# Performance work log

Measured on AMD Instinct MI355X. Metric: run time of the kernel, lower is better.

## Reference

```python
import jax, jax.numpy as jnp
import numpy as np

ALPHA = 0.2  # LeakyReLU negative slope
NEG_PAD = jnp.float32(-2**31)
N, IN_F, OUT_F = 8192, 512, 64


def setup_inputs() -> dict:
    key = jax.random.key(0)
    k1, k2, k3, k4 = jax.random.split(key, 4)
    h = jax.random.normal(k1, (N, IN_F), dtype=jnp.float32)
    adj = jax.random.randint(k2, (N, N), 0, 2, dtype=jnp.int32)
    # xavier_uniform with gain=1.414
    gain = 1.414
    limW = gain * np.sqrt(6.0 / (IN_F + OUT_F))
    W = jax.random.uniform(k3, (IN_F, OUT_F), dtype=jnp.float32, minval=-limW, maxval=limW)
    lima = gain * np.sqrt(6.0 / (2 * OUT_F + 1))
    a = jax.random.uniform(k4, (2 * OUT_F, 1), dtype=jnp.float32, minval=-lima, maxval=lima)
    return {"h": h, "adj": adj, "W": W, "a": a}


def reference(h, adj, W, a):
    Wh = h @ W                                   # [N, F']
    Wh1 = Wh @ a[:OUT_F, :]                      # [N, 1]
    Wh2 = Wh @ a[OUT_F:, :]                      # [N, 1]
    e = jax.nn.leaky_relu(Wh1 + Wh2.T, negative_slope=ALPHA)  # [N, N]
    attention = jnp.where(adj > 0, e, NEG_PAD)
    attention = jax.nn.softmax(attention, axis=1)
    # dropout in eval mode -> identity
    h_prime = attention @ Wh                     # [N, F']
    return jax.nn.elu(h_prime)                   # concat=True branch
```

## Files before the change

### kernel.cpp

```cpp
#include <hip/hip_runtime.h>
#include <cstdint>
#include <cstddef>

#define LRALPHA 0.2f

typedef _Float16 half8 __attribute__((ext_vector_type(8)));
typedef float f32x4 __attribute__((ext_vector_type(4)));

__global__ __launch_bounds__(256) void k1_wh(
    const float* __restrict__ h, const float* __restrict__ W, const float* __restrict__ a,
    _Float16* __restrict__ whT, float* __restrict__ wh1, float* __restrict__ wh2)
{
  __shared__ __align__(16) float h_lds[32][34];
  __shared__ __align__(16) float w_lds[32][64];
  __shared__ __align__(16) _Float16 whT_l[64][32];

  const int t = threadIdx.x;
  const int tx = t & 15, ty = t >> 4;
  const int i0 = blockIdx.x * 32;

  const int hrow = t >> 3, hk4 = (t & 7) * 4;
  const int wk = t >> 3, wc = (t & 7) * 8;

  float acc00 = 0, acc01 = 0, acc02 = 0, acc03 = 0;
  float acc10 = 0, acc11 = 0, acc12 = 0, acc13 = 0;

  float4 hv  = *reinterpret_cast<const float4*>(&h[(size_t)(i0 + hrow) * 512 + hk4]);
  float4 wv0 = *reinterpret_cast<const float4*>(&W[(size_t)wk * 64 + wc]);
  float4 wv1 = *reinterpret_cast<const float4*>(&W[(size_t)wk * 64 + wc + 4]);

  for (int k0 = 0; k0 < 512; k0 += 32) {
    h_lds[hk4 + 0][hrow] = hv.x;
    h_lds[hk4 + 1][hrow] = hv.y;
    h_lds[hk4 + 2][hrow] = hv.z;
    h_lds[hk4 + 3][hrow] = hv.w;
    *reinterpret_cast<float4*>(&w_lds[wk][wc])     = wv0;
    *reinterpret_cast<float4*>(&w_lds[wk][wc + 4]) = wv1;
    __syncthreads();
    if (k0 + 32 < 512) {
      hv  = *reinterpret_cast<const float4*>(&h[(size_t)(i0 + hrow) * 512 + k0 + 32 + hk4]);
      wv0 = *reinterpret_cast<const float4*>(&W[(size_t)(k0 + 32 + wk) * 64 + wc]);
      wv1 = *reinterpret_cast<const float4*>(&W[(size_t)(k0 + 32 + wk) * 64 + wc + 4]);
    }
#pragma unroll
    for (int kk = 0; kk < 32; ++kk) {
      float2 av = *reinterpret_cast<const float2*>(&h_lds[kk][ty * 2]);
      float4 bv = *reinterpret_cast<const float4*>(&w_lds[kk][tx * 4]);
      acc00 += av.x * bv.x; acc01 += av.x * bv.y; acc02 += av.x * bv.z; acc03 += av.x * bv.w;
      acc10 += av.y * bv.x; acc11 += av.y * bv.y; acc12 += av.y * bv.z; acc13 += av.y * bv.w;
    }
    __syncthreads();
  }

  const float a10 = a[tx * 4 + 0], a11 = a[tx * 4 + 1], a12 = a[tx * 4 + 2], a13 = a[tx * 4 + 3];
  const float a20 = a[64 + tx * 4 + 0], a21 = a[64 + tx * 4 + 1], a22 = a[64 + tx * 4 + 2], a23 = a[64 + tx * 4 + 3];
  float s1_0 = acc00 * a10 + acc01 * a11 + acc02 * a12 + acc03 * a13;
  float s1_1 = acc10 * a10 + acc11 * a11 + acc12 * a12 + acc13 * a13;
  float s2_0 = acc00 * a20 + acc01 * a21 + acc02 * a22 + acc03 * a23;
  float s2_1 = acc10 * a20 + acc11 * a21 + acc12 * a22 + acc13 * a23;
#pragma unroll
  for (int m = 1; m < 16; m <<= 1) {
    s1_0 += __shfl_xor(s1_0, m); s1_1 += __shfl_xor(s1_1, m);
    s2_0 += __shfl_xor(s2_0, m); s2_1 += __shfl_xor(s2_1, m);
  }
  if (tx == 0) {
    wh1[i0 + ty * 2 + 0] = s1_0; wh1[i0 + ty * 2 + 1] = s1_1;
    wh2[i0 + ty * 2 + 0] = s2_0; wh2[i0 + ty * 2 + 1] = s2_1;
  }

  whT_l[tx * 4 + 0][ty * 2 + 0] = (_Float16)acc00;
  whT_l[tx * 4 + 1][ty * 2 + 0] = (_Float16)acc01;
  whT_l[tx * 4 + 2][ty * 2 + 0] = (_Float16)acc02;
  whT_l[tx * 4 + 3][ty * 2 + 0] = (_Float16)acc03;
  whT_l[tx * 4 + 0][ty * 2 + 1] = (_Float16)acc10;
  whT_l[tx * 4 + 1][ty * 2 + 1] = (_Float16)acc11;
  whT_l[tx * 4 + 2][ty * 2 + 1] = (_Float16)acc12;
  whT_l[tx * 4 + 3][ty * 2 + 1] = (_Float16)acc13;
  __syncthreads();
  {
    const int c = t >> 2, r8 = (t & 3) * 8;
    half8 v = *reinterpret_cast<const half8*>(&whT_l[c][r8]);
    *reinterpret_cast<half8*>(&whT[(size_t)c * 8192 + i0 + r8]) = v;
  }
}

__global__ __launch_bounds__(256) void k1b_max(const float* __restrict__ wh2,
                                               float* __restrict__ G)
{
  const int t = threadIdx.x;
  float m = -1e30f;
  for (int i = t; i < 8192; i += 256) m = fmaxf(m, wh2[i]);
#pragma unroll
  for (int mask = 32; mask >= 1; mask >>= 1) m = fmaxf(m, __shfl_xor(m, mask));
  __shared__ float wm[4];
  if ((t & 63) == 0) wm[t >> 6] = m;
  __syncthreads();
  if (t == 0) G[0] = fmaxf(fmaxf(wm[0], wm[1]), fmaxf(wm[2], wm[3]));
}

__global__ __launch_bounds__(512) void k2_attn(
    const int* __restrict__ adj, const _Float16* __restrict__ whT,
    const float* __restrict__ wh1, const float* __restrict__ wh2,
    const float* __restrict__ Gp, float* __restrict__ out)
{
  __shared__ __align__(16) unsigned char smraw[16384];
  __shared__ float denom_s[64];
  _Float16* P = reinterpret_cast<_Float16*>(smraw);
  float* O = reinterpret_cast<float*>(smraw);

  const int t = threadIdx.x;
  const int g = t >> 8;
  const int tg = t & 255;
  const int lane = t & 63;
  const int wg = (t >> 6) & 3;
  const int i0 = blockIdx.x * 32;

  if (t < 64) denom_s[t] = 0.f;

  const float Gv = Gp[0];
  const int prow = tg >> 3;
  const int pc8 = tg & 7;
  const float w1r = wh1[i0 + prow];
  const float mx = w1r + Gv;
  const float mh = fmaxf(mx, LRALPHA * mx);
  const int* adj_row = adj + (size_t)(i0 + prow) * 8192 + pc8 * 8;
  const float* wh2o = wh2 + pc8 * 8;

  const int rt = wg >> 1, cp = wg & 1;
  const int arow = rt * 16 + (lane & 15);
  const int kgrp = lane >> 4;
  const _Float16* bbase = whT + (size_t)(cp * 32 + (lane & 15)) * 8192 + kgrp * 8;

  f32x4 acc0 = {0.f, 0.f, 0.f, 0.f}, acc1 = {0.f, 0.f, 0.f, 0.f};

  int4 na0, na1; float4 nw0, nw1;
  {
    const int j0 = g * 64;
    na0 = *reinterpret_cast<const int4*>(adj_row + j0);
    na1 = *reinterpret_cast<const int4*>(adj_row + j0 + 4);
    nw0 = *reinterpret_cast<const float4*>(wh2o + j0);
    nw1 = *reinterpret_cast<const float4*>(wh2o + j0 + 4);
  }
  __syncthreads();

  for (int ci = 0; ci < 64; ++ci) {
    const int j0 = (2 * ci + g) * 64;
    const int buf = ci & 1;
    const int4 a0 = na0, a1 = na1;
    const float4 w0 = nw0, w1v = nw1;

    const _Float16* bp = bbase + j0;
    half8 bf00 = *reinterpret_cast<const half8*>(bp);
    half8 bf01 = *reinterpret_cast<const half8*>(bp + (size_t)16 * 8192);
    half8 bf10 = *reinterpret_cast<const half8*>(bp + 32);
    half8 bf11 = *reinterpret_cast<const half8*>(bp + (size_t)16 * 8192 + 32);

    if (ci < 63) {
      const int jn = (2 * ci + 2 + g) * 64;
      na0 = *reinterpret_cast<const int4*>(adj_row + jn);
      na1 = *reinterpret_cast<const int4*>(adj_row + jn + 4);
      nw0 = *reinterpret_cast<const float4*>(wh2o + jn);
      nw1 = *reinterpret_cast<const float4*>(wh2o + jn + 4);
    }

    half8 pv;
    float ps = 0.f;
#define DO_E(e, AV, WV) { float s_ = w1r + (WV); s_ = fmaxf(s_, LRALPHA * s_); \
    float p_ = ((AV) > 0) ? __expf(s_ - mh) : 0.f; ps += p_; pv[e] = (_Float16)p_; }
    DO_E(0, a0.x, w0.x)  DO_E(1, a0.y, w0.y)  DO_E(2, a0.z, w0.z)  DO_E(3, a0.w, w0.w)
    DO_E(4, a1.x, w1v.x) DO_E(5, a1.y, w1v.y) DO_E(6, a1.z, w1v.z) DO_E(7, a1.w, w1v.w)
#undef DO_E

    float r = ps;
    r += __shfl_xor(r, 1); r += __shfl_xor(r, 2); r += __shfl_xor(r, 4);
    if (pc8 == 0) denom_s[g * 32 + prow] += r;

    {
      const int chunk = pc8 ^ (prow & 7);
      *reinterpret_cast<half8*>(&P[(((g << 1) | buf) << 11) + (prow << 6) + (chunk << 3)]) = pv;
    }
    __syncthreads();

    const int base = (((g << 1) | buf) << 11) + (arow << 6);
    const int cA0 = (kgrp ^ (arow & 7)) << 3;
    const int cA1 = ((4 + kgrp) ^ (arow & 7)) << 3;
    half8 af0 = *reinterpret_cast<const half8*>(&P[base + cA0]);
    half8 af1 = *reinterpret_cast<const half8*>(&P[base + cA1]);
    acc0 = __builtin_amdgcn_mfma_f32_16x16x32_f16(af0, bf00, acc0, 0, 0, 0);
    acc1 = __builtin_amdgcn_mfma_f32_16x16x32_f16(af0, bf01, acc1, 0, 0, 0);
    acc0 = __builtin_amdgcn_mfma_f32_16x16x32_f16(af1, bf10, acc0, 0, 0, 0);
    acc1 = __builtin_amdgcn_mfma_f32_16x16x32_f16(af1, bf11, acc1, 0, 0, 0);
  }

  __syncthreads();
  const int orow = rt * 16 + kgrp * 4;
  const int ocol = cp * 32 + (lane & 15);
  if (g == 0) {
#pragma unroll
    for (int q = 0; q < 4; ++q) {
      O[(orow + q) * 64 + ocol]      = acc0[q];
      O[(orow + q) * 64 + ocol + 16] = acc1[q];
    }
  }
  __syncthreads();
  if (g == 1) {
#pragma unroll
    for (int q = 0; q < 4; ++q) {
      O[(orow + q) * 64 + ocol]      += acc0[q];
      O[(orow + q) * 64 + ocol + 16] += acc1[q];
    }
  }
  __syncthreads();
  {
    const int row = t >> 4, c4 = (t & 15) * 4;
    const float d = denom_s[row] + denom_s[32 + row];
    const float inv = 1.0f / d;
    float4 v = *reinterpret_cast<const float4*>(&O[row * 64 + c4]);
    float4 o;
    o.x = v.x * inv; o.y = v.y * inv; o.z = v.z * inv; o.w = v.w * inv;
    o.x = o.x > 0.f ? o.x : __expf(o.x) - 1.f;
    o.y = o.y > 0.f ? o.y : __expf(o.y) - 1.f;
    o.z = o.z > 0.f ? o.z : __expf(o.z) - 1.f;
    o.w = o.w > 0.f ? o.w : __expf(o.w) - 1.f;
    *reinterpret_cast<float4*>(&out[(size_t)(i0 + row) * 64 + c4]) = o;
  }
}

extern "C" void kernel_launch(void* const* d_in, const int* in_sizes, int n_in,
                              void* d_out, int out_size, void* d_ws, size_t ws_size,
                              hipStream_t stream) {
  const float* h   = (const float*)d_in[0];
  const int*   adj = (const int*)d_in[1];
  const float* W   = (const float*)d_in[2];
  const float* a   = (const float*)d_in[3];
  float* out = (float*)d_out;

  char* ws = (char*)d_ws;
  _Float16* whT = (_Float16*)ws;
  float* wh1 = (float*)(ws + (1 << 20));
  float* wh2 = (float*)(ws + (1 << 20) + 32768);
  float* G   = (float*)(ws + (1 << 20) + 65536);

  k1_wh<<<dim3(256), dim3(256), 0, stream>>>(h, W, a, whT, wh1, wh2);
  k1b_max<<<dim3(1), dim3(256), 0, stream>>>(wh2, G);
  k2_attn<<<dim3(256), dim3(512), 0, stream>>>(adj, whT, wh1, wh2, G, out);
}
```

Baseline: 106.8 us.

## Compute attention probabilities directly in MFMA operand layout, split K across waves

```diff
diff --git a/kernel.cpp b/kernel.cpp
--- a/kernel.cpp
+++ b/kernel.cpp
@@ -98,126 +98,116 @@
   if (t == 0) G[0] = fmaxf(fmaxf(wm[0], wm[1]), fmaxf(wm[2], wm[3]));
 }
 
-__global__ __launch_bounds__(512) void k2_attn(
+__global__ __launch_bounds__(256) void k2_attn(
     const int* __restrict__ adj, const _Float16* __restrict__ whT,
     const float* __restrict__ wh1, const float* __restrict__ wh2,
     const float* __restrict__ Gp, float* __restrict__ out)
 {
-  __shared__ __align__(16) unsigned char smraw[16384];
-  __shared__ float denom_s[64];
-  _Float16* P = reinterpret_cast<_Float16*>(smraw);
-  float* O = reinterpret_cast<float*>(smraw);
+  __shared__ __align__(16) float Osm[4][16][64];
+  __shared__ float Dsm[4][16];
 
   const int t = threadIdx.x;
-  const int g = t >> 8;
-  const int tg = t & 255;
   const int lane = t & 63;
-  const int wg = (t >> 6) & 3;
-  const int i0 = blockIdx.x * 32;
-
-  if (t < 64) denom_s[t] = 0.f;
+  const int w = t >> 6;
+  const int c = lane & 15;
+  const int ks = lane >> 4;
+  const int i0 = blockIdx.x * 16;
 
   const float Gv = Gp[0];
-  const int prow = tg >> 3;
-  const int pc8 = tg & 7;
-  const float w1r = wh1[i0 + prow];
+  const float w1r = wh1[i0 + c];
   const float mx = w1r + Gv;
   const float mh = fmaxf(mx, LRALPHA * mx);
-  const int* adj_row = adj + (size_t)(i0 + prow) * 8192 + pc8 * 8;
-  const float* wh2o = wh2 + pc8 * 8;
-
-  const int rt = wg >> 1, cp = wg & 1;
-  const int arow = rt * 16 + (lane & 15);
-  const int kgrp = lane >> 4;
-  const _Float16* bbase = whT + (size_t)(cp * 32 + (lane & 15)) * 8192 + kgrp * 8;
-
-  f32x4 acc0 = {0.f, 0.f, 0.f, 0.f}, acc1 = {0.f, 0.f, 0.f, 0.f};
-
-  int4 na0, na1; float4 nw0, nw1;
-  {
-    const int j0 = g * 64;
-    na0 = *reinterpret_cast<const int4*>(adj_row + j0);
-    na1 = *reinterpret_cast<const int4*>(adj_row + j0 + 4);
-    nw0 = *reinterpret_cast<const float4*>(wh2o + j0);
-    nw1 = *reinterpret_cast<const float4*>(wh2o + j0 + 4);
+
+  const int*      adjp = adj + (size_t)(i0 + c) * 8192 + w * 2048 + ks * 8;
+  const float*    wh2p = wh2 + w * 2048 + ks * 8;
+  const _Float16* bp0  = whT + (size_t)c * 8192 + w * 2048 + ks * 8;
+  const _Float16* bp1  = bp0 + (size_t)16 * 8192;
+  const _Float16* bp2  = bp0 + (size_t)32 * 8192;
+  const _Float16* bp3  = bp0 + (size_t)48 * 8192;
+
+  f32x4 acc0 = {0.f,0.f,0.f,0.f}, acc1 = {0.f,0.f,0.f,0.f};
+  f32x4 acc2 = {0.f,0.f,0.f,0.f}, acc3 = {0.f,0.f,0.f,0.f};
+  float ps = 0.f;
+
+  int4 Aa0, Aa1, Ba0, Ba1;
+  float4 Aw0, Aw1, Bw0, Bw1;
+  half8 Ab0, Ab1, Ab2, Ab3, Bb0, Bb1, Bb2, Bb3;
+
+#define LOADSET(P, CI) do { const int jj_ = (CI) * 32;                          \
+    P##a0 = *reinterpret_cast<const int4*>(adjp + jj_);                         \
+    P##a1 = *reinterpret_cast<const int4*>(adjp + jj_ + 4);                     \
+    P##w0 = *reinterpret_cast<const float4*>(wh2p + jj_);                       \
+    P##w1 = *reinterpret_cast<const float4*>(wh2p + jj_ + 4);                   \
+    P##b0 = *reinterpret_cast<const half8*>(bp0 + jj_);                         \
+    P##b1 = *reinterpret_cast<const half8*>(bp1 + jj_);                         \
+    P##b2 = *reinterpret_cast<const half8*>(bp2 + jj_);                         \
+    P##b3 = *reinterpret_cast<const half8*>(bp3 + jj_); } while (0)
+
+#define BODY(P, NEXTCI) do {                                                    \
+    const int4 ca0 = P##a0, ca1 = P##a1;                                        \
+    const float4 cw0 = P##w0, cw1 = P##w1;                                      \
+    const half8 cb0 = P##b0, cb1 = P##b1, cb2 = P##b2, cb3 = P##b3;             \
+    if ((NEXTCI) < 64) LOADSET(P, NEXTCI);                                      \
+    half8 af;                                                                   \
+    { float s_ = w1r + cw0.x; s_ = fmaxf(s_, LRALPHA*s_);                       \
+      float p_ = (ca0.x > 0) ? __expf(s_ - mh) : 0.f; ps += p_; af[0] = (_Float16)p_; } \
+    { float s_ = w1r + cw0.y; s_ = fmaxf(s_, LRALPHA*s_);                       \
+      float p_ = (ca0.y > 0) ? __expf(s_ - mh) : 0.f; ps += p_; af[1] = (_Float16)p_; } \
+    { float s_ = w1r + cw0.z; s_ = fmaxf(s_, LRALPHA*s_);                       \
+      float p_ = (ca0.z > 0) ? __expf(s_ - mh) : 0.f; ps += p_; af[2] = (_Float16)p_; } \
+    { float s_ = w1r + cw0.w; s_ = fmaxf(s_, LRALPHA*s_);                       \
+      float p_ = (ca0.w > 0) ? __expf(s_ - mh) : 0.f; ps += p_; af[3] = (_Float16)p_; } \
+    { float s_ = w1r + cw1.x; s_ = fmaxf(s_, LRALPHA*s_);                       \
+      float p_ = (ca1.x > 0) ? __expf(s_ - mh) : 0.f; ps += p_; af[4] = (_Float16)p_; } \
+    { float s_ = w1r + cw1.y; s_ = fmaxf(s_, LRALPHA*s_);                       \
+      float p_ = (ca1.y > 0) ? __expf(s_ - mh) : 0.f; ps += p_; af[5] = (_Float16)p_; } \
+    { float s_ = w1r + cw1.z; s_ = fmaxf(s_, LRALPHA*s_);                       \
+      float p_ = (ca1.z > 0) ? __expf(s_ - mh) : 0.f; ps += p_; af[6] = (_Float16)p_; } \
+    { float s_ = w1r + cw1.w; s_ = fmaxf(s_, LRALPHA*s_);                       \
+      float p_ = (ca1.w > 0) ? __expf(s_ - mh) : 0.f; ps += p_; af[7] = (_Float16)p_; } \
+    acc0 = __builtin_amdgcn_mfma_f32_16x16x32_f16(af, cb0, acc0, 0, 0, 0);      \
+    acc1 = __builtin_amdgcn_mfma_f32_16x16x32_f16(af, cb1, acc1, 0, 0, 0);      \
+    acc2 = __builtin_amdgcn_mfma_f32_16x16x32_f16(af, cb2, acc2, 0, 0, 0);      \
+    acc3 = __builtin_amdgcn_mfma_f32_16x16x32_f16(af, cb3, acc3, 0, 0, 0);      \
+  } while (0)
+
+  LOADSET(A, 0);
+  LOADSET(B, 1);
+
+  for (int ci = 0; ci < 64; ci += 2) {
+    BODY(A, ci + 2);
+    BODY(B, ci + 3);
+  }
+#undef BODY
+#undef LOADSET
+
+  float r = ps;
+  r += __shfl_xor(r, 16);
+  r += __shfl_xor(r, 32);
+  if (ks == 0) Dsm[w][c] = r;
+
+#pragma unroll
+  for (int q = 0; q < 4; ++q) {
+    Osm[w][ks * 4 + q][ 0 + c] = acc0[q];
+    Osm[w][ks * 4 + q][16 + c] = acc1[q];
+    Osm[w][ks * 4 + q][32 + c] = acc2[q];
+    Osm[w][ks * 4 + q][48 + c] = acc3[q];
   }
   __syncthreads();
 
-  for (int ci = 0; ci < 64; ++ci) {
-    const int j0 = (2 * ci + g) * 64;
-    const int buf = ci & 1;
-    const int4 a0 = na0, a1 = na1;
-    const float4 w0 = nw0, w1v = nw1;
-
-    const _Float16* bp = bbase + j0;
-    half8 bf00 = *reinterpret_cast<const half8*>(bp);
-    half8 bf01 = *reinterpret_cast<const half8*>(bp + (size_t)16 * 8192);
-    half8 bf10 = *reinterpret_cast<const half8*>(bp + 32);
-    half8 bf11 = *reinterpret_cast<const half8*>(bp + (size_t)16 * 8192 + 32);
-
-    if (ci < 63) {
-      const int jn = (2 * ci + 2 + g) * 64;
-      na0 = *reinterpret_cast<const int4*>(adj_row + jn);
-      na1 = *reinterpret_cast<const int4*>(adj_row + jn + 4);
-      nw0 = *reinterpret_cast<const float4*>(wh2o + jn);
-      nw1 = *reinterpret_cast<const float4*>(wh2o + jn + 4);
-    }
-
-    half8 pv;
-    float ps = 0.f;
-#define DO_E(e, AV, WV) { float s_ = w1r + (WV); s_ = fmaxf(s_, LRALPHA * s_); \
-    float p_ = ((AV) > 0) ? __expf(s_ - mh) : 0.f; ps += p_; pv[e] = (_Float16)p_; }
-    DO_E(0, a0.x, w0.x)  DO_E(1, a0.y, w0.y)  DO_E(2, a0.z, w0.z)  DO_E(3, a0.w, w0.w)
-    DO_E(4, a1.x, w1v.x) DO_E(5, a1.y, w1v.y) DO_E(6, a1.z, w1v.z) DO_E(7, a1.w, w1v.w)
-#undef DO_E
-
-    float r = ps;
-    r += __shfl_xor(r, 1); r += __shfl_xor(r, 2); r += __shfl_xor(r, 4);
-    if (pc8 == 0) denom_s[g * 32 + prow] += r;
-
-    {
-      const int chunk = pc8 ^ (prow & 7);
-      *reinterpret_cast<half8*>(&P[(((g << 1) | buf) << 11) + (prow << 6) + (chunk << 3)]) = pv;
-    }
-    __syncthreads();
-
-    const int base = (((g << 1) | buf) << 11) + (arow << 6);
-    const int cA0 = (kgrp ^ (arow & 7)) << 3;
-    const int cA1 = ((4 + kgrp) ^ (arow & 7)) << 3;
-    half8 af0 = *reinterpret_cast<const half8*>(&P[base + cA0]);
-    half8 af1 = *reinterpret_cast<const half8*>(&P[base + cA1]);
-    acc0 = __builtin_amdgcn_mfma_f32_16x16x32_f16(af0, bf00, acc0, 0, 0, 0);
-    acc1 = __builtin_amdgcn_mfma_f32_16x16x32_f16(af0, bf01, acc1, 0, 0, 0);
-    acc0 = __builtin_amdgcn_mfma_f32_16x16x32_f16(af1, bf10, acc0, 0, 0, 0);
-    acc1 = __builtin_amdgcn_mfma_f32_16x16x32_f16(af1, bf11, acc1, 0, 0, 0);
-  }
-
-  __syncthreads();
-  const int orow = rt * 16 + kgrp * 4;
-  const int ocol = cp * 32 + (lane & 15);
-  if (g == 0) {
-#pragma unroll
-    for (int q = 0; q < 4; ++q) {
-      O[(orow + q) * 64 + ocol]      = acc0[q];
-      O[(orow + q) * 64 + ocol + 16] = acc1[q];
-    }
-  }
-  __syncthreads();
-  if (g == 1) {
-#pragma unroll
-    for (int q = 0; q < 4; ++q) {
-      O[(orow + q) * 64 + ocol]      += acc0[q];
-      O[(orow + q) * 64 + ocol + 16] += acc1[q];
-    }
-  }
-  __syncthreads();
   {
     const int row = t >> 4, c4 = (t & 15) * 4;
-    const float d = denom_s[row] + denom_s[32 + row];
+    float4 v0 = *reinterpret_cast<const float4*>(&Osm[0][row][c4]);
+    float4 v1 = *reinterpret_cast<const float4*>(&Osm[1][row][c4]);
+    float4 v2 = *reinterpret_cast<const float4*>(&Osm[2][row][c4]);
+    float4 v3 = *reinterpret_cast<const float4*>(&Osm[3][row][c4]);
+    const float d = Dsm[0][row] + Dsm[1][row] + Dsm[2][row] + Dsm[3][row];
     const float inv = 1.0f / d;
-    float4 v = *reinterpret_cast<const float4*>(&O[row * 64 + c4]);
     float4 o;
-    o.x = v.x * inv; o.y = v.y * inv; o.z = v.z * inv; o.w = v.w * inv;
+    o.x = (v0.x + v1.x + v2.x + v3.x) * inv;
+    o.y = (v0.y + v1.y + v2.y + v3.y) * inv;
+    o.z = (v0.z + v1.z + v2.z + v3.z) * inv;
+    o.w = (v0.w + v1.w + v2.w + v3.w) * inv;
     o.x = o.x > 0.f ? o.x : __expf(o.x) - 1.f;
     o.y = o.y > 0.f ? o.y : __expf(o.y) - 1.f;
     o.z = o.z > 0.f ? o.z : __expf(o.z) - 1.f;
@@ -243,5 +233,5 @@
 
   k1_wh<<<dim3(256), dim3(256), 0, stream>>>(h, W, a, whT, wh1, wh2);
   k1b_max<<<dim3(1), dim3(256), 0, stream>>>(wh2, G);
-  k2_attn<<<dim3(256), dim3(512), 0, stream>>>(adj, whT, wh1, wh2, G, out);
-}
+  k2_attn<<<dim3(512), dim3(256), 0, stream>>>(adj, whT, wh1, wh2, G, out);
+}
```

Result: slower. 133.5 us (+25.0%).
